# Optimization experiments

Measured on AMD Instinct MI355X. Metric: run time of the kernel, lower is better.

Reference implementation:

```python
import jax, jax.numpy as jnp
import numpy as np

N, E, D, H, G = 50000, 600000, 128, 128, 128
NEG_SLOPE = 0.01
EPS = 1e-12


def _xavier(key, out_dim, in_dim):
    lim = float(np.sqrt(6.0 / (in_dim + out_dim)))
    return jax.random.uniform(key, (out_dim, in_dim), minval=-lim, maxval=lim, dtype=jnp.float32)


def setup_inputs() -> dict:
    key = jax.random.key(0)
    ks = jax.random.split(key, 12)
    x = jax.random.uniform(ks[0], (N, D), dtype=jnp.float32)
    edge_index = jax.random.randint(ks[1], (2, E), 0, N, dtype=jnp.int64)
    batch = jnp.sort(jax.random.randint(ks[2], (N,), 0, G, dtype=jnp.int64))
    return {
        "x": x,
        "edge_index": edge_index,
        "batch": batch,
        "W1l": _xavier(ks[3], H, D),
        "W1r": _xavier(ks[4], H, D),
        "W2l": _xavier(ks[5], H, H),
        "W2r": _xavier(ks[6], H, H),
        "fc1_W": _xavier(ks[7], H, H + D),
        "fc1_b": jnp.zeros((H,), jnp.float32),
        "fc2_W": _xavier(ks[8], H, H + H),
        "fc2_b": jnp.zeros((H,), jnp.float32),
        "fc3_W": _xavier(ks[9], H, H),
        "fc3_b": jnp.zeros((H,), jnp.float32),
    }


def _leaky(x):
    return jnp.where(x >= 0, x, NEG_SLOPE * x)


def _l2norm(x):
    # torch F.normalize(p=2, dim=-1) with eps clamp
    n = jnp.sqrt(jnp.sum(x * x, axis=-1, keepdims=True))
    return x / jnp.maximum(n, EPS)


def _sage_conv(x, src, dst, Wl, Wr):
    # PyG SAGEConv: out = lin_l(mean_{j in N(i)} x_j) + lin_r(x_i), L2-normalized
    msum = jax.ops.segment_sum(x[src], dst, num_segments=x.shape[0])  # [N, F]
    cnt = jax.ops.segment_sum(jnp.ones_like(dst, dtype=x.dtype), dst, num_segments=x.shape[0])
    mean = msum / jnp.maximum(cnt, 1.0)[:, None]
    out = mean @ Wl.T + x @ Wr.T
    return _l2norm(out)


def _preprocess(x):
    # row-normalize features (1/rowsum, inf -> 0)
    rs = jnp.sum(x, axis=1)
    rinv = jnp.where(rs == 0, 0.0, 1.0 / rs)
    return x * rinv[:, None]


def reference(x, edge_index, batch, W1l, W1r, W2l, W2r, fc1_W, fc1_b, fc2_W, fc2_b, fc3_W, fc3_b):
    src, dst = edge_index[0], edge_index[1]
    x = _preprocess(x)
    x_skip = x
    h = _leaky(_sage_conv(x, src, dst, W1l, W1r))
    h = jnp.concatenate([h, x_skip], axis=1)
    h = _leaky(h @ fc1_W.T + fc1_b)
    # double_layer=True
    h_skip = h
    h2 = _leaky(_sage_conv(h, src, dst, W2l, W2r))
    h2 = jnp.concatenate([h2, h_skip], axis=1)
    h = _leaky(h2 @ fc2_W.T + fc2_b)
    # global_add_pool over graphs
    pooled = jax.ops.segment_sum(h, batch, num_segments=G)  # [G, H]
    out = _leaky(pooled @ fc3_W.T + fc3_b)
    return _l2norm(out)
```

## Files before the change

kernel.cpp:

```cpp
#include <hip/hip_runtime.h>
#include <hip/hip_bf16.h>


#define NEG_SLOPE 0.01f
#define L2EPS 1e-12f

typedef unsigned short u16;
typedef short bf16x8 __attribute__((ext_vector_type(8)));
typedef short s16x4  __attribute__((ext_vector_type(4)));
typedef float f32x4  __attribute__((ext_vector_type(4)));

__device__ __forceinline__ float bf_lo(unsigned int u) {
    union { unsigned int i; float f; } v; v.i = u << 16; return v.f;
}
__device__ __forceinline__ float bf_hi(unsigned int u) {
    union { unsigned int i; float f; } v; v.i = u & 0xffff0000u; return v.f;
}
__device__ __forceinline__ u16 f2bf(float f) {
    union { float f; unsigned int i; } v; v.f = f;
    unsigned int r = v.i + 0x7fffu + ((v.i >> 16) & 1u);
    return (u16)(r >> 16);
}
__device__ __forceinline__ float bf2f(u16 u) {
    union { unsigned int i; float f; } v; v.i = ((unsigned int)u) << 16; return v.f;
}

__global__ void k_preprocess(const float* __restrict__ x, u16* __restrict__ xp, int N) {
    int node = blockIdx.x * 4 + (threadIdx.x >> 6);
    int lane = threadIdx.x & 63;
    if (node >= N) return;
    float2 v = ((const float2*)x)[(size_t)node * 64 + lane];
    float s = v.x + v.y;
    #pragma unroll
    for (int off = 32; off > 0; off >>= 1) s += __shfl_xor(s, off);
    float rinv = (s == 0.0f) ? 0.0f : 1.0f / s;
    unsigned int lo = f2bf(v.x * rinv), hi = f2bf(v.y * rinv);
    ((unsigned int*)xp)[(size_t)node * 64 + lane] = lo | (hi << 16);
}

__global__ void k_wconv(const float* __restrict__ W1l, const float* __restrict__ W1r,
                        const float* __restrict__ W2l, const float* __restrict__ W2r,
                        const float* __restrict__ f1,  const float* __restrict__ f2,
                        u16* __restrict__ wbf) {
    int i = blockIdx.x * 256 + threadIdx.x;
    if (i >= 32768) return;
    int e = i * 4;
    const float* src; int off;
    if (e < 65536) {
        int m = e >> 14; off = e & 16383;
        src = (m == 0) ? W1l : (m == 1) ? W1r : (m == 2) ? W2l : W2r;
    } else {
        int m = (e - 65536) >> 15; off = (e - 65536) & 32767;
        src = (m == 0) ? f1 : f2;
    }
    float4 v = *(const float4*)(src + off);
    uint2 o;
    o.x = (unsigned int)f2bf(v.x) | ((unsigned int)f2bf(v.y) << 16);
    o.y = (unsigned int)f2bf(v.z) | ((unsigned int)f2bf(v.w) << 16);
    *(uint2*)(wbf + e) = o;
}

__global__ void k_deg(const int* __restrict__ ei, int* __restrict__ deg, int E) {
    int e = blockIdx.x * blockDim.x + threadIdx.x;
    if (e >= E) return;
    atomicAdd(&deg[ei[E + e]], 1);
}

__global__ void k_scan_part(const int* __restrict__ deg, int* __restrict__ rs,
                            int* __restrict__ bsum, int N) {
    __shared__ int wsum[16];
    int t = threadIdx.x;
    int lane = t & 63, w = t >> 6;
    int i = blockIdx.x * 1024 + t;
    int v = (i < N) ? deg[i] : 0;
    int s = v;
    #pragma unroll
    for (int off = 1; off < 64; off <<= 1) {
        int u = __shfl_up(s, off);
        if (lane >= off) s += u;
    }
    if (lane == 63) wsum[w] = s;
    __syncthreads();
    if (w == 0) {
        int x = (lane < 16) ? wsum[lane] : 0;
        #pragma unroll
        for (int off = 1; off < 16; off <<= 1) {
            int u = __shfl_up(x, off);
            if (lane >= off) x += u;
        }
        if (lane < 16) wsum[lane] = x;
    }
    __syncthreads();
    int wexcl = (w == 0) ? 0 : wsum[w - 1];
    if (i < N) rs[i] = wexcl + s - v;
    if (t == 1023) bsum[blockIdx.x] = wexcl + s;
}

__global__ void k_scan_bsum(int* __restrict__ bsum, int* __restrict__ rs,
                            int nb, int N) {
    int lane = threadIdx.x;
    int v = (lane < nb) ? bsum[lane] : 0;
    int s = v;
    #pragma unroll
    for (int off = 1; off < 64; off <<= 1) {
        int u = __shfl_up(s, off);
        if (lane >= off) s += u;
    }
    if (lane < nb) bsum[lane] = s - v;
    if (lane == nb - 1) rs[N] = s;
}

__global__ void k_scan_add(int* __restrict__ rs, int* __restrict__ cursor,
                           const int* __restrict__ bsum, int N) {
    int i = blockIdx.x * 256 + threadIdx.x;
    if (i >= N) return;
    int v = rs[i] + bsum[i >> 10];
    rs[i] = v;
    cursor[i] = v;
}

__global__ void k_fill(const int* __restrict__ ei, int* __restrict__ cursor,
                       int* __restrict__ csr, int E) {
    int e = blockIdx.x * blockDim.x + threadIdx.x;
    if (e >= E) return;
    int src = ei[e];
    int dst = ei[E + e];
    int pos = atomicAdd(&cursor[dst], 1);
    csr[pos] = src;
}

__global__ void k_agg(const u16* __restrict__ feat, const int* __restrict__ csr,
                      const int* __restrict__ rs, u16* __restrict__ mean, int N) {
    int node = blockIdx.x * 4 + (threadIdx.x >> 6);
    int lane = threadIdx.x & 63;
    if (node >= N) return;
    int beg = rs[node], end = rs[node + 1];
    int d = end - beg;
    int q   = lane >> 4;
    int sub = lane & 15;
    const uint4* fp = (const uint4*)feat;
    float4 aA0 = {0.f,0.f,0.f,0.f}, aB0 = {0.f,0.f,0.f,0.f};
    float4 aA1 = {0.f,0.f,0.f,0.f}, aB1 = {0.f,0.f,0.f,0.f};
    int p = beg + q;
    for (; p + 4 < end; p += 8) {
        int s0 = csr[p], s1 = csr[p + 4];
        uint4 v0 = fp[(size_t)s0 * 16 + sub];
        uint4 v1 = fp[(size_t)s1 * 16 + sub];
        aA0.x += bf_lo(v0.x); aA0.y += bf_hi(v0.x);
        aA0.z += bf_lo(v0.y); aA0.w += bf_hi(v0.y);
        aB0.x += bf_lo(v0.z); aB0.y += bf_hi(v0.z);
        aB0.z += bf_lo(v0.w); aB0.w += bf_hi(v0.w);
        aA1.x += bf_lo(v1.x); aA1.y += bf_hi(v1.x);
        aA1.z += bf_lo(v1.y); aA1.w += bf_hi(v1.y);
        aB1.x += bf_lo(v1.z); aB1.y += bf_hi(v1.z);
        aB1.z += bf_lo(v1.w); aB1.w += bf_hi(v1.w);
    }
    if (p < end) {
        int s0 = csr[p];
        uint4 v0 = fp[(size_t)s0 * 16 + sub];
        aA0.x += bf_lo(v0.x); aA0.y += bf_hi(v0.x);
        aA0.z += bf_lo(v0.y); aA0.w += bf_hi(v0.y);
        aB0.x += bf_lo(v0.z); aB0.y += bf_hi(v0.z);
        aB0.z += bf_lo(v0.w); aB0.w += bf_hi(v0.w);
    }
    aA0.x += aA1.x; aA0.y += aA1.y; aA0.z += aA1.z; aA0.w += aA1.w;
    aB0.x += aB1.x; aB0.y += aB1.y; aB0.z += aB1.z; aB0.w += aB1.w;
    #pragma unroll
    for (int off = 16; off <= 32; off <<= 1) {
        aA0.x += __shfl_xor(aA0.x, off); aA0.y += __shfl_xor(aA0.y, off);
        aA0.z += __shfl_xor(aA0.z, off); aA0.w += __shfl_xor(aA0.w, off);
        aB0.x += __shfl_xor(aB0.x, off); aB0.y += __shfl_xor(aB0.y, off);
        aB0.z += __shfl_xor(aB0.z, off); aB0.w += __shfl_xor(aB0.w, off);
    }
    if (q == 0) {
        float inv = (d > 0) ? (1.0f / (float)d) : 0.0f;
        uint4 o;
        o.x = (unsigned int)f2bf(aA0.x * inv) | ((unsigned int)f2bf(aA0.y * inv) << 16);
        o.y = (unsigned int)f2bf(aA0.z * inv) | ((unsigned int)f2bf(aA0.w * inv) << 16);
        o.z = (unsigned int)f2bf(aB0.x * inv) | ((unsigned int)f2bf(aB0.y * inv) << 16);
        o.w = (unsigned int)f2bf(aB0.z * inv) | ((unsigned int)f2bf(aB0.w * inv) << 16);
        ((uint4*)mean)[(size_t)node * 16 + sub] = o;
    }
}


#define LOAD_T1(kb_) do {                                                      \
    const u16* As_ = ((kb_) < 4) ? Am : Ax;                                    \
    const u16* Ws_ = ((kb_) < 4) ? Wlb : Wrb;                                  \
    int kl_ = ((kb_) & 3) * 32;                                                \
    int gr_ = i0 + a_row;                                                      \
    if (gr_ < N) sA = *(const uint4*)(As_ + (size_t)gr_ * 128 + kl_ + a_q * 8);\
    else         sA = make_uint4(0u, 0u, 0u, 0u);                              \
    const u16* wp_ = Ws_ + (size_t)w_row * 128 + kl_ + w_half * 16;            \
    sw0 = *(const uint4*)(wp_);  sw1 = *(const uint4*)(wp_ + 8);               \
} while (0)

#define LOAD_T2(kb_) do {                                                      \
    int kl_ = ((kb_) & 3) * 32;                                                \
    if ((kb_) >= 4) {                                                          \
        int gr_ = i0 + a_row;                                                  \
        if (gr_ < N) sA = *(const uint4*)(Ax + (size_t)gr_ * 128 + kl_ + a_q * 8); \
        else         sA = make_uint4(0u, 0u, 0u, 0u);                          \
    }                                                                          \
    int ko_ = kl_ + (((kb_) >= 4) ? 128 : 0);                                  \
    const u16* wp_ = Wfb + (size_t)w_row * 256 + ko_ + w_half * 16;            \
    sw0 = *(const uint4*)(wp_);  sw1 = *(const uint4*)(wp_ + 8);               \
} while (0)

#define STORE_A() do { *(uint4*)&Al[a_half][a_row][a_col0] = sA; } while (0)
#define STORE_W() do {                                                         \
    *(uint4*)&Wl[w_half][w_row][0] = sw0;                                      \
    *(uint4*)&Wl[w_half][w_row][8] = sw1;                                      \
} while (0)

__global__ __launch_bounds__(256, 3) void k_layer(
    const u16* __restrict__ Am, const u16* __restrict__ Ax,
    const u16* __restrict__ Wlb, const u16* __restrict__ Wrb,
    const u16* __restrict__ Wfb, const float* __restrict__ bias,
    u16* __restrict__ out, int N)
{
    __shared__ u16 Al[2][64][40];
    __shared__ u16 Wl[2][128][40];
    __shared__ u16 hT[64][136];
    int t = threadIdx.x;
    int i0 = blockIdx.x * 64;

    int a_row  = t >> 2;
    int a_q    = t & 3;
    int a_half = a_q >> 1;
    int a_col0 = (a_q & 1) * 8;
    int w_row  = t >> 1;
    int w_half = t & 1;

    int c16 = t & 15;
    int g   = (t >> 4) & 3;
    int wid = t >> 6;
    int ar  = wid * 16 + c16;
    int g4  = g * 4;

    f32x4 acc[8];
    #pragma unroll
    for (int cb = 0; cb < 8; ++cb) acc[cb] = (f32x4){0.f, 0.f, 0.f, 0.f};

    uint4 sA, sw0, sw1;
    union U8 { bf16x8 v; s16x4 h[2]; };

    LOAD_T1(0);
    for (int kb = 0; kb < 8; ++kb) {
        __syncthreads();
        STORE_A(); STORE_W();
        __syncthreads();
        if (kb < 7) LOAD_T1(kb + 1);

        U8 af;
        af.h[0] = *(const s16x4*)&Al[0][ar][g4];
        af.h[1] = *(const s16x4*)&Al[1][ar][g4];
        #pragma unroll
        for (int cb = 0; cb < 8; ++cb) {
            U8 bfr;
            int wr = cb * 16 + c16;
            bfr.h[0] = *(const s16x4*)&Wl[0][wr][g4];
            bfr.h[1] = *(const s16x4*)&Wl[1][wr][g4];
            acc[cb] = __builtin_amdgcn_mfma_f32_16x16x32_bf16(af.v, bfr.v, acc[cb], 0, 0, 0);
        }
    }

    {
        float s0 = 0.f, s1 = 0.f, s2 = 0.f, s3 = 0.f;
        #pragma unroll
        for (int cb = 0; cb < 8; ++cb) {
            s0 += acc[cb][0] * acc[cb][0];
            s1 += acc[cb][1] * acc[cb][1];
            s2 += acc[cb][2] * acc[cb][2];
            s3 += acc[cb][3] * acc[cb][3];
        }
        #pragma unroll
        for (int off = 1; off < 16; off <<= 1) {
            s0 += __shfl_xor(s0, off);
            s1 += __shfl_xor(s1, off);
            s2 += __shfl_xor(s2, off);
            s3 += __shfl_xor(s3, off);
        }
        float scs[4];
        scs[0] = 1.0f / fmaxf(sqrtf(s0), L2EPS);
        scs[1] = 1.0f / fmaxf(sqrtf(s1), L2EPS);
        scs[2] = 1.0f / fmaxf(sqrtf(s2), L2EPS);
        scs[3] = 1.0f / fmaxf(sqrtf(s3), L2EPS);
        #pragma unroll
        for (int reg = 0; reg < 4; ++reg) {
            int rl = wid * 16 + g * 4 + reg;
            #pragma unroll
            for (int cb = 0; cb < 8; ++cb) {
                float xv = acc[cb][reg] * scs[reg];
                float r = (xv >= 0.f) ? xv : NEG_SLOPE * xv;
                hT[rl][cb * 16 + c16] = f2bf(r);
            }
        }
    }

    #pragma unroll
    for (int cb = 0; cb < 8; ++cb) acc[cb] = (f32x4){0.f, 0.f, 0.f, 0.f};

    LOAD_T2(0);
    for (int kb = 0; kb < 8; ++kb) {
        __syncthreads();
        if (kb >= 4) STORE_A();
        STORE_W();
        __syncthreads();
        if (kb < 7) LOAD_T2(kb + 1);

        U8 af;
        if (kb < 4) {
            af.h[0] = *(const s16x4*)&hT[ar][kb * 32 + g4];
            af.h[1] = *(const s16x4*)&hT[ar][kb * 32 + 16 + g4];
        } else {
            af.h[0] = *(const s16x4*)&Al[0][ar][g4];
            af.h[1] = *(const s16x4*)&Al[1][ar][g4];
        }
        #pragma unroll
        for (int cb = 0; cb < 8; ++cb) {
            U8 bfr;
            int wr = cb * 16 + c16;
            bfr.h[0] = *(const s16x4*)&Wl[0][wr][g4];
            bfr.h[1] = *(const s16x4*)&Wl[1][wr][g4];
            acc[cb] = __builtin_amdgcn_mfma_f32_16x16x32_bf16(af.v, bfr.v, acc[cb], 0, 0, 0);
        }
    }

    float bv[8];
    #pragma unroll
    for (int cb = 0; cb < 8; ++cb) bv[cb] = bias[cb * 16 + c16];
    int rbase = i0 + wid * 16 + g * 4;
    #pragma unroll
    for (int reg = 0; reg < 4; ++reg) {
        int grow = rbase + reg;
        if (grow >= N) continue;
        #pragma unroll
        for (int cb = 0; cb < 8; ++cb) {
            float xv = acc[cb][reg] + bv[cb];
            float r = (xv >= 0.f) ? xv : NEG_SLOPE * xv;
            out[(size_t)grow * 128 + cb * 16 + c16] = f2bf(r);
        }
    }
}

#define POOL_ROWS 128
__global__ void k_pool(const u16* __restrict__ h3, const int* __restrict__ batch,
                       float* __restrict__ pooled, int N) {
    int f = threadIdx.x;
    int base = blockIdx.x * POOL_ROWS;
    if (base >= N) return;
    int end = min(base + POOL_ROWS, N);
    float acc = 0.f;
    int cur = batch[base];
    for (int i = base; i < end; ++i) {
        int g = batch[i];
        if (g != cur) {
            atomicAdd(&pooled[cur * 128 + f], acc);
            acc = 0.f; cur = g;
        }
        acc += bf2f(h3[(size_t)i * 128 + f]);
    }
    atomicAdd(&pooled[cur * 128 + f], acc);
}

__global__ void k_fc3(const float* __restrict__ pooled, const float* __restrict__ W,
                      const float* __restrict__ b, float* __restrict__ out) {
    int g = blockIdx.x, f = threadIdx.x;
    __shared__ float prow[128];
    __shared__ float red[128];
    prow[f] = pooled[g * 128 + f];
    __syncthreads();
    float acc = b[f];
    #pragma unroll 8
    for (int k = 0; k < 128; ++k) acc += prow[k] * W[f * 128 + k];
    float v = (acc >= 0.f) ? acc : NEG_SLOPE * acc;
    red[f] = v * v;
    __syncthreads();
    for (int o = 64; o > 0; o >>= 1) {
        if (f < o) red[f] += red[f + o];
        __syncthreads();
    }
    float sc = 1.0f / fmaxf(sqrtf(red[0]), L2EPS);
    out[g * 128 + f] = v * sc;
}

extern "C" void kernel_launch(void* const* d_in, const int* in_sizes, int n_in,
                              void* d_out, int out_size, void* d_ws, size_t ws_size,
                              hipStream_t stream) {
    const float* x    = (const float*)d_in[0];
    const int*   ei   = (const int*)d_in[1];
    const int*   batch= (const int*)d_in[2];
    const float* W1l  = (const float*)d_in[3];
    const float* W1r  = (const float*)d_in[4];
    const float* W2l  = (const float*)d_in[5];
    const float* W2r  = (const float*)d_in[6];
    const float* fc1W = (const float*)d_in[7];
    const float* fc1b = (const float*)d_in[8];
    const float* fc2W = (const float*)d_in[9];
    const float* fc2b = (const float*)d_in[10];
    const float* fc3W = (const float*)d_in[11];
    const float* fc3b = (const float*)d_in[12];

    int N = in_sizes[0] / 128;
    int E = in_sizes[1] / 2;
    int G = out_size / 128;
    float* out = (float*)d_out;

    char* ws = (char*)d_ws;
    size_t off = 0;
    auto alloc = [&](size_t bytes) -> void* {
        void* p = ws + off;
        off = (off + bytes + 255) & ~(size_t)255;
        return p;
    };
    u16* xp     = (u16*)alloc((size_t)N * 128 * 2);
    u16* mean   = (u16*)alloc((size_t)N * 128 * 2);
    u16* h1     = (u16*)alloc((size_t)N * 128 * 2);
    u16* wbf    = (u16*)alloc(131072 * 2);
    float* pooled = (float*)alloc((size_t)G * 128 * 4);
    int* deg    = (int*)alloc((size_t)N * 4);
    int* rs     = (int*)alloc((size_t)(N + 1) * 4);
    int* cursor = (int*)alloc((size_t)N * 4);
    int* csr    = (int*)alloc((size_t)E * 4);
    int* bsum   = (int*)alloc(64 * 4);
    (void)ws_size; (void)n_in;

    hipMemsetAsync(deg, 0, (size_t)N * 4, stream);
    hipMemsetAsync(pooled, 0, (size_t)G * 128 * 4, stream);

    int nb = (N + 1023) / 1024;
    k_preprocess<<<(N + 3) / 4, 256, 0, stream>>>(x, xp, N);
    k_wconv<<<128, 256, 0, stream>>>(W1l, W1r, W2l, W2r, fc1W, fc2W, wbf);
    k_deg<<<(E + 255) / 256, 256, 0, stream>>>(ei, deg, E);
    k_scan_part<<<nb, 1024, 0, stream>>>(deg, rs, bsum, N);
    k_scan_bsum<<<1, 64, 0, stream>>>(bsum, rs, nb, N);
    k_scan_add<<<(N + 255) / 256, 256, 0, stream>>>(rs, cursor, bsum, N);
    k_fill<<<(E + 255) / 256, 256, 0, stream>>>(ei, cursor, csr, E);

    int gb = (N + 63) / 64;
    k_agg<<<(N + 3) / 4, 256, 0, stream>>>(xp, csr, rs, mean, N);
    k_layer<<<gb, 256, 0, stream>>>(
        mean, xp, wbf, wbf + 16384, wbf + 65536, fc1b, h1, N);

    k_agg<<<(N + 3) / 4, 256, 0, stream>>>(h1, csr, rs, mean, N);
    k_layer<<<gb, 256, 0, stream>>>(
        mean, h1, wbf + 32768, wbf + 49152, wbf + 98304, fc2b, xp, N);

    k_pool<<<(N + POOL_ROWS - 1) / POOL_ROWS, 128, 0, stream>>>(xp, batch, pooled, N);
    k_fc3<<<G, 128, 0, stream>>>(pooled, fc3W, fc3b, out);
}
```

Measured before the change: 315.7 us.

## Halve k_layer block to 128 threads with two 16-row MFMA tiles per wave

The fused layer kernel now runs 2 waves per 64-row block instead of 4. Each wave computes two 16-row output tiles, so every weight fragment read from LDS feeds two MFMAs. The staging loads are reorganised so each thread moves more data per k-step. This aims to halve LDS weight traffic per MFMA and cut thread overhead, at the cost of doubled accumulator registers and fewer waves per block to hide latency.

```diff
diff --git a/kernel.cpp b/kernel.cpp
--- a/kernel.cpp
+++ b/kernel.cpp
@@ -189,31 +189,40 @@
     const u16* Ws_ = ((kb_) < 4) ? Wlb : Wrb;                                  \
     int kl_ = ((kb_) & 3) * 32;                                                \
     int gr_ = i0 + a_row;                                                      \
-    if (gr_ < N) sA = *(const uint4*)(As_ + (size_t)gr_ * 128 + kl_ + a_q * 8);\
-    else         sA = make_uint4(0u, 0u, 0u, 0u);                              \
-    const u16* wp_ = Ws_ + (size_t)w_row * 128 + kl_ + w_half * 16;            \
-    sw0 = *(const uint4*)(wp_);  sw1 = *(const uint4*)(wp_ + 8);               \
+    if (gr_ < N) {                                                             \
+        const u16* ap_ = As_ + (size_t)gr_ * 128 + kl_ + a_half * 16;          \
+        sa0 = *(const uint4*)(ap_);  sa1 = *(const uint4*)(ap_ + 8);           \
+    } else { sa0 = make_uint4(0u,0u,0u,0u); sa1 = sa0; }                       \
+    const u16* wp_ = Ws_ + (size_t)t * 128 + kl_;                              \
+    sw0 = *(const uint4*)(wp_);       sw1 = *(const uint4*)(wp_ + 8);          \
+    sw2 = *(const uint4*)(wp_ + 16);  sw3 = *(const uint4*)(wp_ + 24);         \
 } while (0)
 
 #define LOAD_T2(kb_) do {                                                      \
     int kl_ = ((kb_) & 3) * 32;                                                \
     if ((kb_) >= 4) {                                                          \
         int gr_ = i0 + a_row;                                                  \
-        if (gr_ < N) sA = *(const uint4*)(Ax + (size_t)gr_ * 128 + kl_ + a_q * 8); \
-        else         sA = make_uint4(0u, 0u, 0u, 0u);                          \
+        if (gr_ < N) {                                                         \
+            const u16* ap_ = Ax + (size_t)gr_ * 128 + kl_ + a_half * 16;       \
+            sa0 = *(const uint4*)(ap_);  sa1 = *(const uint4*)(ap_ + 8);       \
+        } else { sa0 = make_uint4(0u,0u,0u,0u); sa1 = sa0; }                   \
     }                                                                          \
     int ko_ = kl_ + (((kb_) >= 4) ? 128 : 0);                                  \
-    const u16* wp_ = Wfb + (size_t)w_row * 256 + ko_ + w_half * 16;            \
-    sw0 = *(const uint4*)(wp_);  sw1 = *(const uint4*)(wp_ + 8);               \
+    const u16* wp_ = Wfb + (size_t)t * 256 + ko_;                              \
+    sw0 = *(const uint4*)(wp_);       sw1 = *(const uint4*)(wp_ + 8);          \
+    sw2 = *(const uint4*)(wp_ + 16);  sw3 = *(const uint4*)(wp_ + 24);         \
 } while (0)
 
-#define STORE_A() do { *(uint4*)&Al[a_half][a_row][a_col0] = sA; } while (0)
+#define STORE_A() do {                                                         \
+    *(uint4*)&Al[a_half][a_row][0] = sa0;                                      \
+    *(uint4*)&Al[a_half][a_row][8] = sa1;                                      \
+} while (0)
 #define STORE_W() do {                                                         \
-    *(uint4*)&Wl[w_half][w_row][0] = sw0;                                      \
-    *(uint4*)&Wl[w_half][w_row][8] = sw1;                                      \
+    *(uint4*)&Wl[0][t][0] = sw0;  *(uint4*)&Wl[0][t][8] = sw1;                 \
+    *(uint4*)&Wl[1][t][0] = sw2;  *(uint4*)&Wl[1][t][8] = sw3;                 \
 } while (0)
 
-__global__ __launch_bounds__(256, 3) void k_layer(
+__global__ __launch_bounds__(128) void k_layer(
     const u16* __restrict__ Am, const u16* __restrict__ Ax,
     const u16* __restrict__ Wlb, const u16* __restrict__ Wrb,
     const u16* __restrict__ Wfb, const float* __restrict__ bias,
@@ -225,24 +234,24 @@
     int t = threadIdx.x;
     int i0 = blockIdx.x * 64;
 
-    int a_row  = t >> 2;
-    int a_q    = t & 3;
-    int a_half = a_q >> 1;
-    int a_col0 = (a_q & 1) * 8;
-    int w_row  = t >> 1;
-    int w_half = t & 1;
+    int a_row  = t >> 1;
+    int a_half = t & 1;
 
     int c16 = t & 15;
     int g   = (t >> 4) & 3;
     int wid = t >> 6;
-    int ar  = wid * 16 + c16;
+    int ar0 = wid * 32 + c16;
+    int ar1 = ar0 + 16;
     int g4  = g * 4;
 
-    f32x4 acc[8];
-    #pragma unroll
-    for (int cb = 0; cb < 8; ++cb) acc[cb] = (f32x4){0.f, 0.f, 0.f, 0.f};
-
-    uint4 sA, sw0, sw1;
+    f32x4 acc0[8], acc1[8];
+    #pragma unroll
+    for (int cb = 0; cb < 8; ++cb) {
+        acc0[cb] = (f32x4){0.f, 0.f, 0.f, 0.f};
+        acc1[cb] = (f32x4){0.f, 0.f, 0.f, 0.f};
+    }
+
+    uint4 sa0, sa1, sw0, sw1, sw2, sw3;
     union U8 { bf16x8 v; s16x4 h[2]; };
 
     LOAD_T1(0);
@@ -252,54 +261,72 @@
         __syncthreads();
         if (kb < 7) LOAD_T1(kb + 1);
 
-        U8 af;
-        af.h[0] = *(const s16x4*)&Al[0][ar][g4];
-        af.h[1] = *(const s16x4*)&Al[1][ar][g4];
+        U8 af0, af1;
+        af0.h[0] = *(const s16x4*)&Al[0][ar0][g4];
+        af0.h[1] = *(const s16x4*)&Al[1][ar0][g4];
+        af1.h[0] = *(const s16x4*)&Al[0][ar1][g4];
+        af1.h[1] = *(const s16x4*)&Al[1][ar1][g4];
         #pragma unroll
         for (int cb = 0; cb < 8; ++cb) {
             U8 bfr;
             int wr = cb * 16 + c16;
             bfr.h[0] = *(const s16x4*)&Wl[0][wr][g4];
             bfr.h[1] = *(const s16x4*)&Wl[1][wr][g4];
-            acc[cb] = __builtin_amdgcn_mfma_f32_16x16x32_bf16(af.v, bfr.v, acc[cb], 0, 0, 0);
+            acc0[cb] = __builtin_amdgcn_mfma_f32_16x16x32_bf16(af0.v, bfr.v, acc0[cb], 0, 0, 0);
+            acc1[cb] = __builtin_amdgcn_mfma_f32_16x16x32_bf16(af1.v, bfr.v, acc1[cb], 0, 0, 0);
         }
     }
 
     {
         float s0 = 0.f, s1 = 0.f, s2 = 0.f, s3 = 0.f;
+        float u0 = 0.f, u1 = 0.f, u2 = 0.f, u3 = 0.f;
         #pragma unroll
         for (int cb = 0; cb < 8; ++cb) {
-            s0 += acc[cb][0] * acc[cb][0];
-            s1 += acc[cb][1] * acc[cb][1];
-            s2 += acc[cb][2] * acc[cb][2];
-            s3 += acc[cb][3] * acc[cb][3];
+            s0 += acc0[cb][0] * acc0[cb][0];
+            s1 += acc0[cb][1] * acc0[cb][1];
+            s2 += acc0[cb][2] * acc0[cb][2];
+            s3 += acc0[cb][3] * acc0[cb][3];
+            u0 += acc1[cb][0] * acc1[cb][0];
+            u1 += acc1[cb][1] * acc1[cb][1];
+            u2 += acc1[cb][2] * acc1[cb][2];
+            u3 += acc1[cb][3] * acc1[cb][3];
         }
         #pragma unroll
         for (int off = 1; off < 16; off <<= 1) {
-            s0 += __shfl_xor(s0, off);
-            s1 += __shfl_xor(s1, off);
-            s2 += __shfl_xor(s2, off);
-            s3 += __shfl_xor(s3, off);
-        }
-        float scs[4];
-        scs[0] = 1.0f / fmaxf(sqrtf(s0), L2EPS);
-        scs[1] = 1.0f / fmaxf(sqrtf(s1), L2EPS);
-        scs[2] = 1.0f / fmaxf(sqrtf(s2), L2EPS);
-        scs[3] = 1.0f / fmaxf(sqrtf(s3), L2EPS);
+            s0 += __shfl_xor(s0, off); s1 += __shfl_xor(s1, off);
+            s2 += __shfl_xor(s2, off); s3 += __shfl_xor(s3, off);
+            u0 += __shfl_xor(u0, off); u1 += __shfl_xor(u1, off);
+            u2 += __shfl_xor(u2, off); u3 += __shfl_xor(u3, off);
+        }
+        float scs0[4], scs1[4];
+        scs0[0] = 1.0f / fmaxf(sqrtf(s0), L2EPS);
+        scs0[1] = 1.0f / fmaxf(sqrtf(s1), L2EPS);
+        scs0[2] = 1.0f / fmaxf(sqrtf(s2), L2EPS);
+        scs0[3] = 1.0f / fmaxf(sqrtf(s3), L2EPS);
+        scs1[0] = 1.0f / fmaxf(sqrtf(u0), L2EPS);
+        scs1[1] = 1.0f / fmaxf(sqrtf(u1), L2EPS);
+        scs1[2] = 1.0f / fmaxf(sqrtf(u2), L2EPS);
+        scs1[3] = 1.0f / fmaxf(sqrtf(u3), L2EPS);
         #pragma unroll
         for (int reg = 0; reg < 4; ++reg) {
-            int rl = wid * 16 + g * 4 + reg;
+            int rl0 = wid * 32 + g * 4 + reg;
             #pragma unroll
             for (int cb = 0; cb < 8; ++cb) {
-                float xv = acc[cb][reg] * scs[reg];
+                float xv = acc0[cb][reg] * scs0[reg];
                 float r = (xv >= 0.f) ? xv : NEG_SLOPE * xv;
-                hT[rl][cb * 16 + c16] = f2bf(r);
+                hT[rl0][cb * 16 + c16] = f2bf(r);
+                float yv = acc1[cb][reg] * scs1[reg];
+                float q = (yv >= 0.f) ? yv : NEG_SLOPE * yv;
+                hT[rl0 + 16][cb * 16 + c16] = f2bf(q);
             }
         }
     }
 
     #pragma unroll
-    for (int cb = 0; cb < 8; ++cb) acc[cb] = (f32x4){0.f, 0.f, 0.f, 0.f};
+    for (int cb = 0; cb < 8; ++cb) {
+        acc0[cb] = (f32x4){0.f, 0.f, 0.f, 0.f};
+        acc1[cb] = (f32x4){0.f, 0.f, 0.f, 0.f};
+    }
 
     LOAD_T2(0);
     for (int kb = 0; kb < 8; ++kb) {
@@ -309,13 +336,17 @@
         __syncthreads();
         if (kb < 7) LOAD_T2(kb + 1);
 
-        U8 af;
+        U8 af0, af1;
         if (kb < 4) {
-            af.h[0] = *(const s16x4*)&hT[ar][kb * 32 + g4];
-            af.h[1] = *(const s16x4*)&hT[ar][kb * 32 + 16 + g4];
+            af0.h[0] = *(const s16x4*)&hT[ar0][kb * 32 + g4];
+            af0.h[1] = *(const s16x4*)&hT[ar0][kb * 32 + 16 + g4];
+            af1.h[0] = *(const s16x4*)&hT[ar1][kb * 32 + g4];
+            af1.h[1] = *(const s16x4*)&hT[ar1][kb * 32 + 16 + g4];
         } else {
-            af.h[0] = *(const s16x4*)&Al[0][ar][g4];
-            af.h[1] = *(const s16x4*)&Al[1][ar][g4];
+            af0.h[0] = *(const s16x4*)&Al[0][ar0][g4];
+            af0.h[1] = *(const s16x4*)&Al[1][ar0][g4];
+            af1.h[0] = *(const s16x4*)&Al[0][ar1][g4];
+            af1.h[1] = *(const s16x4*)&Al[1][ar1][g4];
         }
         #pragma unroll
         for (int cb = 0; cb < 8; ++cb) {
@@ -323,23 +354,34 @@
             int wr = cb * 16 + c16;
             bfr.h[0] = *(const s16x4*)&Wl[0][wr][g4];
             bfr.h[1] = *(const s16x4*)&Wl[1][wr][g4];
-            acc[cb] = __builtin_amdgcn_mfma_f32_16x16x32_bf16(af.v, bfr.v, acc[cb], 0, 0, 0);
+            acc0[cb] = __builtin_amdgcn_mfma_f32_16x16x32_bf16(af0.v, bfr.v, acc0[cb], 0, 0, 0);
+            acc1[cb] = __builtin_amdgcn_mfma_f32_16x16x32_bf16(af1.v, bfr.v, acc1[cb], 0, 0, 0);
         }
     }
 
     float bv[8];
     #pragma unroll
     for (int cb = 0; cb < 8; ++cb) bv[cb] = bias[cb * 16 + c16];
-    int rbase = i0 + wid * 16 + g * 4;
+    int rbase = i0 + wid * 32 + g * 4;
     #pragma unroll
     for (int reg = 0; reg < 4; ++reg) {
-        int grow = rbase + reg;
-        if (grow >= N) continue;
-        #pragma unroll
-        for (int cb = 0; cb < 8; ++cb) {
-            float xv = acc[cb][reg] + bv[cb];
-            float r = (xv >= 0.f) ? xv : NEG_SLOPE * xv;
-            out[(size_t)grow * 128 + cb * 16 + c16] = f2bf(r);
+        int gr0 = rbase + reg;
+        if (gr0 < N) {
+            #pragma unroll
+            for (int cb = 0; cb < 8; ++cb) {
+                float xv = acc0[cb][reg] + bv[cb];
+                float r = (xv >= 0.f) ? xv : NEG_SLOPE * xv;
+                out[(size_t)gr0 * 128 + cb * 16 + c16] = f2bf(r);
+            }
+        }
+        int gr1 = rbase + 16 + reg;
+        if (gr1 < N) {
+            #pragma unroll
+            for (int cb = 0; cb < 8; ++cb) {
+                float yv = acc1[cb][reg] + bv[cb];
+                float q = (yv >= 0.f) ? yv : NEG_SLOPE * yv;
+                out[(size_t)gr1 * 128 + cb * 16 + c16] = f2bf(q);
+            }
         }
     }
 }
@@ -440,11 +482,11 @@
 
     int gb = (N + 63) / 64;
     k_agg<<<(N + 3) / 4, 256, 0, stream>>>(xp, csr, rs, mean, N);
-    k_layer<<<gb, 256, 0, stream>>>(
+    k_layer<<<gb, 128, 0, stream>>>(
         mean, xp, wbf, wbf + 16384, wbf + 65536, fc1b, h1, N);
 
     k_agg<<<(N + 3) / 4, 256, 0, stream>>>(h1, csr, rs, mean, N);
-    k_layer<<<gb, 256, 0, stream>>>(
+    k_layer<<<gb, 128, 0, stream>>>(
         mean, h1, wbf + 32768, wbf + 49152, wbf + 98304, fc2b, xp, N);
 
     k_pool<<<(N + POOL_ROWS - 1) / POOL_ROWS, 128, 0, stream>>>(xp, batch, pooled, N);
```

New measurement: 325.1 us. 3.0% more time.
